# Kernel optimization log

Hardware: AMD Instinct MI355X
Metric: run time of the kernel (lower is better)

The kernel has to match this reference:

```python
import jax, jax.numpy as jnp
import numpy as np

NHEADS = 8
EPS = 1e-6


def setup_inputs() -> dict:
    key = jax.random.key(0)
    ks = jax.random.split(key, 6)
    B, N, H, W = 4, 80, 24, 24
    hidden, guid = 128, 128
    n = B * H * W
    S = 77
    return {
        "query": jax.random.normal(ks[0], (B, N, H, W, hidden + guid), jnp.float32),
        "x": jax.random.normal(ks[1], (n, S, hidden), jnp.float32),
        "guidance": jax.random.normal(ks[2], (n, S, guid), jnp.float32),
        "Wq": jax.random.normal(ks[3], (hidden + guid, hidden), jnp.float32) * (1.0 / np.sqrt(hidden + guid)),
        "bq": jnp.zeros((hidden,), jnp.float32),
        "Wk": jax.random.normal(ks[4], (hidden + guid, hidden), jnp.float32) * (1.0 / np.sqrt(hidden + guid)),
        "bk": jnp.zeros((hidden,), jnp.float32),
        "Wv": jax.random.normal(ks[5], (hidden, hidden), jnp.float32) * (1.0 / np.sqrt(hidden)),
        "bv": jnp.zeros((hidden,), jnp.float32),
    }


def _feature_map(x):
    return jax.nn.elu(x) + 1.0


def reference(query, x, guidance, Wq, bq, Wk, bk, Wv, bv):
    B, N, H, W, C = query.shape
    Dh = Wq.shape[1] // NHEADS  # head dim
    # 'B N H W C -> (B H W) N C'
    qin = query.transpose(0, 2, 3, 1, 4).reshape(B * H * W, N, C)
    q = qin @ Wq + bq                                   # (n, N, hidden)
    k = jnp.concatenate([x, guidance], axis=-1) @ Wk + bk  # (n, S, hidden)
    v = x @ Wv + bv                                     # (n, S, hidden)
    n, S = v.shape[0], v.shape[1]
    q = q.reshape(n, N, NHEADS, Dh)
    k = k.reshape(n, S, NHEADS, Dh)
    v = v.reshape(n, S, NHEADS, Dh)
    Q = _feature_map(q)
    K = _feature_map(k)
    v_scaled = v / S
    KV = jnp.einsum('nshd,nshv->nhdv', K, v_scaled)     # (n, h, d, d)
    Z = 1.0 / (jnp.einsum('nlhd,nhd->nlh', Q, K.sum(axis=1)) + EPS)
    queried = jnp.einsum('nlhd,nhdv,nlh->nlhv', Q, KV, Z) * S  # (n, N, h, d)
    out = queried.mean(axis=1).reshape(n, NHEADS * Dh)  # (n, hidden)
    return out.reshape(B, H, W, NHEADS * Dh)
```

## Files before the change

### kernel.cpp

```cpp
#include <hip/hip_runtime.h>
#include <hip/hip_bf16.h>

typedef __attribute__((ext_vector_type(8))) short bf16x8;
typedef __attribute__((ext_vector_type(4))) float f32x4;

#define S77  77
#define NQ   80
#define CS   136
#define KS2  104

#define MFMA(a,b,c) __builtin_amdgcn_mfma_f32_16x16x32_bf16((a),(b),(c),0,0,0)

__device__ __forceinline__ unsigned int cvt_pk(float a, float b) {
    union { __hip_bfloat162 h; unsigned int u; } c;
    c.h = __float22bfloat162_rn(make_float2(a, b));
    return c.u;
}
__device__ __forceinline__ unsigned short f2bf(float f) {
    union { __hip_bfloat16 h; unsigned short u; } c;
    c.h = __float2bfloat16(f);
    return c.u;
}

__global__ void transpose_weights(const float* __restrict__ Wq,
                                  const float* __restrict__ Wk,
                                  const float* __restrict__ Wv,
                                  unsigned short* __restrict__ ws) {
    int t = blockIdx.x * 256 + threadIdx.x;
    if (t < 32768) {
        int k = t >> 7, c = t & 127;
        ws[c * 256 + k] = f2bf(Wq[t]);
    } else if (t < 65536) {
        int u = t - 32768; int k = u >> 7, c = u & 127;
        ws[32768 + c * 256 + k] = f2bf(Wk[u]);
    } else if (t < 81920) {
        int u = t - 65536; int k = u >> 7, c = u & 127;
        ws[65536 + c * 128 + k] = f2bf(Wv[u]);
    }
}

__global__ __launch_bounds__(512, 4)
void attn_kernel(const float* __restrict__ query,
                 const float* __restrict__ x,
                 const float* __restrict__ guid,
                 const unsigned short* __restrict__ wT,
                 const float* __restrict__ bq,
                 const float* __restrict__ bk,
                 const float* __restrict__ bv,
                 float* __restrict__ out)
{
    const int n    = blockIdx.x;
    const int tid  = threadIdx.x;
    const int wid  = tid >> 6;
    const int lane = tid & 63;
    const int quad = lane >> 4;
    const int mr   = lane & 15;
    const int rg   = wid >> 2;
    const int cg   = wid & 3;
    const int b    = n / 576;
    const int hw   = n % 576;
    const int r0   = rg * 48;

    __shared__ union {
        unsigned short stage[2][96 * CS];
        unsigned short tr[2][128 * KS2];
        float qbar[256];
    } U;
    __shared__ float KsumP[256];

    const unsigned short* WqT = wT;
    const unsigned short* WkT = wT + 32768;
    const unsigned short* WvT = wT + 65536;
    const f32x4 cZ = {0.f, 0.f, 0.f, 0.f};

    const float* xg = x    + (size_t)n * S77 * 128;
    const float* gg = guid + (size_t)n * S77 * 128;

    const int srow = tid >> 5;
    const int seg  = tid & 31;

    float4 sb[5];

    f32x4 Kacc[3][2], Vacc[3][2];
    #pragma unroll
    for (int i = 0; i < 3; ++i) {
        Kacc[i][0] = cZ; Kacc[i][1] = cZ;
        Vacc[i][0] = cZ; Vacc[i][1] = cZ;
    }

    #pragma unroll
    for (int it = 0; it < 5; ++it) {
        const int s = srow + it * 16;
        if (s < S77) sb[it] = *(const float4*)(xg + (size_t)s * 128 + seg * 4);
    }
    #pragma unroll
    for (int it = 0; it < 5; ++it) {
        const int s = srow + it * 16;
        if (s < S77) {
            uint2 p; p.x = cvt_pk(sb[it].x, sb[it].y); p.y = cvt_pk(sb[it].z, sb[it].w);
            *(uint2*)&U.stage[0][s * CS + seg * 4] = p;
        }
    }
    __syncthreads();

    #pragma unroll
    for (int c = 0; c < 2; ++c) {
        if (c == 0) {
            #pragma unroll
            for (int it = 0; it < 5; ++it) {
                const int s = srow + it * 16;
                if (s < S77) sb[it] = *(const float4*)(gg + (size_t)s * 128 + seg * 4);
            }
        }
        const unsigned short* sbase = U.stage[c];
        #pragma unroll
        for (int kk = 0; kk < 4; ++kk) {
            const int kloc  = kk * 32 + quad * 8;
            const int kglob = c * 128 + kk * 32;
            bf16x8 a0 = *(const bf16x8*)&sbase[(r0      + mr) * CS + kloc];
            bf16x8 a1 = *(const bf16x8*)&sbase[(r0 + 16 + mr) * CS + kloc];
            bf16x8 a2;
            if (rg == 0) a2 = *(const bf16x8*)&sbase[(32 + mr) * CS + kloc];
            #pragma unroll
            for (int t = 0; t < 2; ++t) {
                const int cc = cg * 32 + t * 16 + mr;
                bf16x8 bkf = *(const bf16x8*)(WkT + cc * 256 + kglob + quad * 8);
                Kacc[0][t] = MFMA(a0, bkf, Kacc[0][t]);
                Kacc[1][t] = MFMA(a1, bkf, Kacc[1][t]);
                if (rg == 0) Kacc[2][t] = MFMA(a2, bkf, Kacc[2][t]);
                if (c == 0) {
                    bf16x8 bvf = *(const bf16x8*)(WvT + cc * 128 + kglob + quad * 8);
                    Vacc[0][t] = MFMA(a0, bvf, Vacc[0][t]);
                    Vacc[1][t] = MFMA(a1, bvf, Vacc[1][t]);
                    if (rg == 0) Vacc[2][t] = MFMA(a2, bvf, Vacc[2][t]);
                }
            }
        }
        if (c == 0) {
            #pragma unroll
            for (int it = 0; it < 5; ++it) {
                const int s = srow + it * 16;
                if (s < S77) {
                    uint2 p; p.x = cvt_pk(sb[it].x, sb[it].y); p.y = cvt_pk(sb[it].z, sb[it].w);
                    *(uint2*)&U.stage[1][s * CS + seg * 4] = p;
                }
            }
        }
        __syncthreads();
    }

    #pragma unroll
    for (int t = 0; t < 2; ++t) {
        const int cc = cg * 32 + t * 16 + mr;
        const float biask = bk[cc];
        const float biasv = bv[cc];
        float ksp = 0.f;
        #pragma unroll
        for (int mt = 0; mt < 3; ++mt) {
            const int s0 = r0 + mt * 16 + quad * 4;
            float kv4[4], vv4[4];
            #pragma unroll
            for (int r = 0; r < 4; ++r) {
                const int s = s0 + r;
                float tk = 0.f, tv = 0.f;
                if (s < S77) {
                    tk = Kacc[mt][t][r] + biask;
                    tk = (tk > 0.f) ? (tk + 1.f) : __expf(tk);
                    tv = Vacc[mt][t][r] + biasv;
                }
                kv4[r] = tk; vv4[r] = tv; ksp += tk;
            }
            uint2 pk_; pk_.x = cvt_pk(kv4[0], kv4[1]); pk_.y = cvt_pk(kv4[2], kv4[3]);
            *(uint2*)&U.tr[0][cc * KS2 + s0] = pk_;
            uint2 pv_; pv_.x = cvt_pk(vv4[0], vv4[1]); pv_.y = cvt_pk(vv4[2], vv4[3]);
            *(uint2*)&U.tr[1][cc * KS2 + s0] = pv_;
        }
        ksp += __shfl_xor(ksp, 16);
        ksp += __shfl_xor(ksp, 32);
        if (quad == 0) KsumP[rg * 128 + cc] = ksp;
    }

    #pragma unroll
    for (int it = 0; it < 5; ++it) {
        const int l = srow + it * 16;
        sb[it] = *(const float4*)(query + ((size_t)(b * 80 + l) * 576 + hw) * 256 + seg * 4);
    }
    __syncthreads();

    f32x4 KVacc = cZ;
    #pragma unroll
    for (int ks3 = 0; ks3 < 3; ++ks3) {
        const int sc = ks3 * 32 + quad * 8;
        bf16x8 a  = *(const bf16x8*)&U.tr[0][(wid * 16 + mr) * KS2 + sc];
        bf16x8 bb = *(const bf16x8*)&U.tr[1][(wid * 16 + mr) * KS2 + sc];
        KVacc = MFMA(a, bb, KVacc);
    }
    __syncthreads();

    f32x4 Qacc[3][2];
    #pragma unroll
    for (int i = 0; i < 3; ++i) { Qacc[i][0] = cZ; Qacc[i][1] = cZ; }

    #pragma unroll
    for (int it = 0; it < 5; ++it) {
        const int l = srow + it * 16;
        uint2 p; p.x = cvt_pk(sb[it].x, sb[it].y); p.y = cvt_pk(sb[it].z, sb[it].w);
        *(uint2*)&U.stage[0][l * CS + seg * 4] = p;
    }
    __syncthreads();

    #pragma unroll
    for (int c = 0; c < 2; ++c) {
        if (c == 0) {
            #pragma unroll
            for (int it = 0; it < 5; ++it) {
                const int l = srow + it * 16;
                sb[it] = *(const float4*)(query + ((size_t)(b * 80 + l) * 576 + hw) * 256 + 128 + seg * 4);
            }
        }
        const unsigned short* sbase = U.stage[c];
        #pragma unroll
        for (int kk = 0; kk < 4; ++kk) {
            const int kloc  = kk * 32 + quad * 8;
            const int kglob = c * 128 + kk * 32;
            bf16x8 a0 = *(const bf16x8*)&sbase[(r0      + mr) * CS + kloc];
            bf16x8 a1 = *(const bf16x8*)&sbase[(r0 + 16 + mr) * CS + kloc];
            bf16x8 a2;
            if (rg == 0) a2 = *(const bf16x8*)&sbase[(32 + mr) * CS + kloc];
            #pragma unroll
            for (int t = 0; t < 2; ++t) {
                const int cc = cg * 32 + t * 16 + mr;
                bf16x8 bqf = *(const bf16x8*)(WqT + cc * 256 + kglob + quad * 8);
                Qacc[0][t] = MFMA(a0, bqf, Qacc[0][t]);
                Qacc[1][t] = MFMA(a1, bqf, Qacc[1][t]);
                if (rg == 0) Qacc[2][t] = MFMA(a2, bqf, Qacc[2][t]);
            }
        }
        if (c == 0) {
            #pragma unroll
            for (int it = 0; it < 5; ++it) {
                const int l = srow + it * 16;
                uint2 p; p.x = cvt_pk(sb[it].x, sb[it].y); p.y = cvt_pk(sb[it].z, sb[it].w);
                *(uint2*)&U.stage[1][l * CS + seg * 4] = p;
            }
        }
        __syncthreads();
    }

    #pragma unroll
    for (int t = 0; t < 2; ++t) {
        const int cc = cg * 32 + t * 16 + mr;
        const float biasq = bq[cc];
        const float ksc = KsumP[cc] + KsumP[128 + cc];
        float qb = 0.f;
        #pragma unroll
        for (int mt = 0; mt < 3; ++mt) {
            if (!(rg == 1 && mt == 2)) {
                #pragma unroll
                for (int r = 0; r < 4; ++r) {
                    float qv = Qacc[mt][t][r] + biasq;
                    qv = (qv > 0.f) ? (qv + 1.f) : __expf(qv);
                    float den = qv * ksc;
                    den += __shfl_xor(den, 1);
                    den += __shfl_xor(den, 2);
                    den += __shfl_xor(den, 4);
                    den += __shfl_xor(den, 8);
                    qb += qv * (1.f / (den + 1e-6f));
                }
            }
        }
        qb += __shfl_xor(qb, 16);
        qb += __shfl_xor(qb, 32);
        if (quad == 0) U.qbar[rg * 128 + cc] = qb;
    }
    __syncthreads();

    {
        float o = 0.f;
        #pragma unroll
        for (int r = 0; r < 4; ++r) {
            const int d = wid * 16 + quad * 4 + r;
            const float qbar = U.qbar[d] + U.qbar[128 + d];
            o += qbar * KVacc[r];
        }
        o += __shfl_xor(o, 16);
        o += __shfl_xor(o, 32);
        if (quad == 0) out[(size_t)n * 128 + wid * 16 + mr] = o * (1.f / 80.f);
    }
}

extern "C" void kernel_launch(void* const* d_in, const int* in_sizes, int n_in,
                              void* d_out, int out_size, void* d_ws, size_t ws_size,
                              hipStream_t stream) {
    const float* query = (const float*)d_in[0];
    const float* x     = (const float*)d_in[1];
    const float* g     = (const float*)d_in[2];
    const float* Wq    = (const float*)d_in[3];
    const float* bq    = (const float*)d_in[4];
    const float* Wk    = (const float*)d_in[5];
    const float* bk    = (const float*)d_in[6];
    const float* Wv    = (const float*)d_in[7];
    const float* bv    = (const float*)d_in[8];
    float* out = (float*)d_out;
    unsigned short* ws = (unsigned short*)d_ws;

    hipLaunchKernelGGL(transpose_weights, dim3(320), dim3(256), 0, stream, Wq, Wk, Wv, ws);
    hipLaunchKernelGGL(attn_kernel, dim3(2304), dim3(512), 0, stream,
                       query, x, g, ws, bq, bk, bv, out);
}
```

Before: 465.9 us.

## Assign one head per wave and transpose K/V fragments in registers

Work is repartitioned so each of the 8 waves owns one 16-column head across all 80 rows, instead of splitting rows and columns across waves. The K/V transpose for the KV matmul now uses cross-lane shuffles rather than an LDS round trip, and the key sums, qbar and output reductions stay within the wave. This removes the tr/qbar/KsumP shared buffers and several __syncthreads, and weight fragments are preloaded into registers. The cost is more register pressure from 5 row tiles per wave and extra shuffle work.

New measurement: 439.5 us. 1.06x faster.

```diff
diff --git a/kernel.cpp b/kernel.cpp
--- a/kernel.cpp
+++ b/kernel.cpp
@@ -4,10 +4,8 @@
 typedef __attribute__((ext_vector_type(8))) short bf16x8;
 typedef __attribute__((ext_vector_type(4))) float f32x4;
 
-#define S77  77
-#define NQ   80
-#define CS   136
-#define KS2  104
+#define S77 77
+#define CS  136
 
 #define MFMA(a,b,c) __builtin_amdgcn_mfma_f32_16x16x32_bf16((a),(b),(c),0,0,0)
 
@@ -39,6 +37,27 @@
     }
 }
 
+__device__ __forceinline__ bf16x8 xpose_frag(const float t0[4], const float t1[4],
+                                             int quad, int mr) {
+    unsigned int pk[4];
+    #pragma unroll
+    for (int r = 0; r < 4; ++r) pk[r] = cvt_pk(t0[r], t1[r]);
+    const int sb0 = ((quad & 1) * 2) * 16 + mr;
+    unsigned int g0[4], g1[4];
+    #pragma unroll
+    for (int r = 0; r < 4; ++r) {
+        g0[r] = __shfl(pk[r], sb0);
+        g1[r] = __shfl(pk[r], sb0 + 16);
+    }
+    const unsigned int sh = (quad & 2) ? 16u : 0u;
+    union { unsigned int u[4]; bf16x8 v; } o;
+    o.u[0] = ((g0[0] >> sh) & 0xffffu) | (((g0[1] >> sh) & 0xffffu) << 16);
+    o.u[1] = ((g0[2] >> sh) & 0xffffu) | (((g0[3] >> sh) & 0xffffu) << 16);
+    o.u[2] = ((g1[0] >> sh) & 0xffffu) | (((g1[1] >> sh) & 0xffffu) << 16);
+    o.u[3] = ((g1[2] >> sh) & 0xffffu) | (((g1[3] >> sh) & 0xffffu) << 16);
+    return o.v;
+}
+
 __global__ __launch_bounds__(512, 4)
 void attn_kernel(const float* __restrict__ query,
                  const float* __restrict__ x,
@@ -51,22 +70,14 @@
 {
     const int n    = blockIdx.x;
     const int tid  = threadIdx.x;
-    const int wid  = tid >> 6;
+    const int h    = tid >> 6;
     const int lane = tid & 63;
     const int quad = lane >> 4;
     const int mr   = lane & 15;
-    const int rg   = wid >> 2;
-    const int cg   = wid & 3;
     const int b    = n / 576;
     const int hw   = n % 576;
-    const int r0   = rg * 48;
-
-    __shared__ union {
-        unsigned short stage[2][96 * CS];
-        unsigned short tr[2][128 * KS2];
-        float qbar[256];
-    } U;
-    __shared__ float KsumP[256];
+
+    __shared__ unsigned short stage[2][80 * CS];
 
     const unsigned short* WqT = wT;
     const unsigned short* WkT = wT + 32768;
@@ -75,19 +86,20 @@
 
     const float* xg = x    + (size_t)n * S77 * 128;
     const float* gg = guid + (size_t)n * S77 * 128;
-
     const int srow = tid >> 5;
     const int seg  = tid & 31;
 
+    const int cc = h * 16 + mr;
+    const float bk_c = bk[cc], bv_c = bv[cc], bq_c = bq[cc];
+
+    bf16x8 wk0[4], wv0[4];
+    #pragma unroll
+    for (int kk = 0; kk < 4; ++kk) {
+        wk0[kk] = *(const bf16x8*)(WkT + cc * 256 + kk * 32 + quad * 8);
+        wv0[kk] = *(const bf16x8*)(WvT + cc * 128 + kk * 32 + quad * 8);
+    }
+
     float4 sb[5];
-
-    f32x4 Kacc[3][2], Vacc[3][2];
-    #pragma unroll
-    for (int i = 0; i < 3; ++i) {
-        Kacc[i][0] = cZ; Kacc[i][1] = cZ;
-        Vacc[i][0] = cZ; Vacc[i][1] = cZ;
-    }
-
     #pragma unroll
     for (int it = 0; it < 5; ++it) {
         const int s = srow + it * 16;
@@ -98,195 +110,162 @@
         const int s = srow + it * 16;
         if (s < S77) {
             uint2 p; p.x = cvt_pk(sb[it].x, sb[it].y); p.y = cvt_pk(sb[it].z, sb[it].w);
-            *(uint2*)&U.stage[0][s * CS + seg * 4] = p;
-        }
-    }
-    __syncthreads();
-
-    #pragma unroll
-    for (int c = 0; c < 2; ++c) {
-        if (c == 0) {
-            #pragma unroll
-            for (int it = 0; it < 5; ++it) {
-                const int s = srow + it * 16;
-                if (s < S77) sb[it] = *(const float4*)(gg + (size_t)s * 128 + seg * 4);
+            *(uint2*)&stage[0][s * CS + seg * 4] = p;
+        }
+    }
+    #pragma unroll
+    for (int it = 0; it < 5; ++it) {
+        const int s = srow + it * 16;
+        if (s < S77) sb[it] = *(const float4*)(gg + (size_t)s * 128 + seg * 4);
+    }
+    __syncthreads();
+
+    f32x4 Kacc[5], Vacc[5];
+    #pragma unroll
+    for (int m = 0; m < 5; ++m) { Kacc[m] = cZ; Vacc[m] = cZ; }
+    #pragma unroll
+    for (int kk = 0; kk < 4; ++kk)
+        #pragma unroll
+        for (int m = 0; m < 5; ++m) {
+            bf16x8 a = *(const bf16x8*)&stage[0][(m * 16 + mr) * CS + kk * 32 + quad * 8];
+            Kacc[m] = MFMA(a, wk0[kk], Kacc[m]);
+            Vacc[m] = MFMA(a, wv0[kk], Vacc[m]);
+        }
+
+    bf16x8 wk1[4];
+    #pragma unroll
+    for (int kk = 0; kk < 4; ++kk)
+        wk1[kk] = *(const bf16x8*)(WkT + cc * 256 + 128 + kk * 32 + quad * 8);
+
+    #pragma unroll
+    for (int it = 0; it < 5; ++it) {
+        const int s = srow + it * 16;
+        if (s < S77) {
+            uint2 p; p.x = cvt_pk(sb[it].x, sb[it].y); p.y = cvt_pk(sb[it].z, sb[it].w);
+            *(uint2*)&stage[1][s * CS + seg * 4] = p;
+        }
+    }
+    #pragma unroll
+    for (int it = 0; it < 5; ++it) {
+        const int l = srow + it * 16;
+        sb[it] = *(const float4*)(query + ((size_t)(b * 80 + l) * 576 + hw) * 256 + seg * 4);
+    }
+    __syncthreads();
+
+    #pragma unroll
+    for (int kk = 0; kk < 4; ++kk)
+        #pragma unroll
+        for (int m = 0; m < 5; ++m) {
+            bf16x8 a = *(const bf16x8*)&stage[1][(m * 16 + mr) * CS + kk * 32 + quad * 8];
+            Kacc[m] = MFMA(a, wk1[kk], Kacc[m]);
+        }
+
+    float kf[5][4], vs[5][4];
+    float ksum = 0.f;
+    #pragma unroll
+    for (int m = 0; m < 5; ++m)
+        #pragma unroll
+        for (int r = 0; r < 4; ++r) {
+            const int s = m * 16 + quad * 4 + r;
+            float tk = 0.f, tv = 0.f;
+            if (s < S77) {
+                tk = Kacc[m][r] + bk_c;
+                tk = (tk > 0.f) ? (tk + 1.f) : __expf(tk);
+                tv = Vacc[m][r] + bv_c;
             }
-        }
-        const unsigned short* sbase = U.stage[c];
-        #pragma unroll
-        for (int kk = 0; kk < 4; ++kk) {
-            const int kloc  = kk * 32 + quad * 8;
-            const int kglob = c * 128 + kk * 32;
-            bf16x8 a0 = *(const bf16x8*)&sbase[(r0      + mr) * CS + kloc];
-            bf16x8 a1 = *(const bf16x8*)&sbase[(r0 + 16 + mr) * CS + kloc];
-            bf16x8 a2;
-            if (rg == 0) a2 = *(const bf16x8*)&sbase[(32 + mr) * CS + kloc];
-            #pragma unroll
-            for (int t = 0; t < 2; ++t) {
-                const int cc = cg * 32 + t * 16 + mr;
-                bf16x8 bkf = *(const bf16x8*)(WkT + cc * 256 + kglob + quad * 8);
-                Kacc[0][t] = MFMA(a0, bkf, Kacc[0][t]);
-                Kacc[1][t] = MFMA(a1, bkf, Kacc[1][t]);
-                if (rg == 0) Kacc[2][t] = MFMA(a2, bkf, Kacc[2][t]);
-                if (c == 0) {
-                    bf16x8 bvf = *(const bf16x8*)(WvT + cc * 128 + kglob + quad * 8);
-                    Vacc[0][t] = MFMA(a0, bvf, Vacc[0][t]);
-                    Vacc[1][t] = MFMA(a1, bvf, Vacc[1][t]);
-                    if (rg == 0) Vacc[2][t] = MFMA(a2, bvf, Vacc[2][t]);
-                }
-            }
-        }
-        if (c == 0) {
-            #pragma unroll
-            for (int it = 0; it < 5; ++it) {
-                const int s = srow + it * 16;
-                if (s < S77) {
-                    uint2 p; p.x = cvt_pk(sb[it].x, sb[it].y); p.y = cvt_pk(sb[it].z, sb[it].w);
-                    *(uint2*)&U.stage[1][s * CS + seg * 4] = p;
-                }
-            }
-        }
-        __syncthreads();
-    }
-
-    #pragma unroll
-    for (int t = 0; t < 2; ++t) {
-        const int cc = cg * 32 + t * 16 + mr;
-        const float biask = bk[cc];
-        const float biasv = bv[cc];
-        float ksp = 0.f;
-        #pragma unroll
-        for (int mt = 0; mt < 3; ++mt) {
-            const int s0 = r0 + mt * 16 + quad * 4;
-            float kv4[4], vv4[4];
-            #pragma unroll
-            for (int r = 0; r < 4; ++r) {
-                const int s = s0 + r;
-                float tk = 0.f, tv = 0.f;
-                if (s < S77) {
-                    tk = Kacc[mt][t][r] + biask;
-                    tk = (tk > 0.f) ? (tk + 1.f) : __expf(tk);
-                    tv = Vacc[mt][t][r] + biasv;
-                }
-                kv4[r] = tk; vv4[r] = tv; ksp += tk;
-            }
-            uint2 pk_; pk_.x = cvt_pk(kv4[0], kv4[1]); pk_.y = cvt_pk(kv4[2], kv4[3]);
-            *(uint2*)&U.tr[0][cc * KS2 + s0] = pk_;
-            uint2 pv_; pv_.x = cvt_pk(vv4[0], vv4[1]); pv_.y = cvt_pk(vv4[2], vv4[3]);
-            *(uint2*)&U.tr[1][cc * KS2 + s0] = pv_;
-        }
-        ksp += __shfl_xor(ksp, 16);
-        ksp += __shfl_xor(ksp, 32);
-        if (quad == 0) KsumP[rg * 128 + cc] = ksp;
-    }
-
-    #pragma unroll
-    for (int it = 0; it < 5; ++it) {
-        const int l = srow + it * 16;
-        sb[it] = *(const float4*)(query + ((size_t)(b * 80 + l) * 576 + hw) * 256 + seg * 4);
-    }
-    __syncthreads();
-
+            kf[m][r] = tk; vs[m][r] = tv; ksum += tk;
+        }
+    ksum += __shfl_xor(ksum, 16);
+    ksum += __shfl_xor(ksum, 32);
+
+    const float z4[4] = {0.f, 0.f, 0.f, 0.f};
     f32x4 KVacc = cZ;
-    #pragma unroll
-    for (int ks3 = 0; ks3 < 3; ++ks3) {
-        const int sc = ks3 * 32 + quad * 8;
-        bf16x8 a  = *(const bf16x8*)&U.tr[0][(wid * 16 + mr) * KS2 + sc];
-        bf16x8 bb = *(const bf16x8*)&U.tr[1][(wid * 16 + mr) * KS2 + sc];
-        KVacc = MFMA(a, bb, KVacc);
-    }
-    __syncthreads();
-
-    f32x4 Qacc[3][2];
-    #pragma unroll
-    for (int i = 0; i < 3; ++i) { Qacc[i][0] = cZ; Qacc[i][1] = cZ; }
+    {
+        bf16x8 af, bf;
+        af = xpose_frag(kf[0], kf[1], quad, mr);
+        bf = xpose_frag(vs[0], vs[1], quad, mr);
+        KVacc = MFMA(af, bf, KVacc);
+        af = xpose_frag(kf[2], kf[3], quad, mr);
+        bf = xpose_frag(vs[2], vs[3], quad, mr);
+        KVacc = MFMA(af, bf, KVacc);
+        af = xpose_frag(kf[4], z4, quad, mr);
+        bf = xpose_frag(vs[4], z4, quad, mr);
+        KVacc = MFMA(af, bf, KVacc);
+    }
 
     #pragma unroll
     for (int it = 0; it < 5; ++it) {
         const int l = srow + it * 16;
         uint2 p; p.x = cvt_pk(sb[it].x, sb[it].y); p.y = cvt_pk(sb[it].z, sb[it].w);
-        *(uint2*)&U.stage[0][l * CS + seg * 4] = p;
-    }
-    __syncthreads();
-
-    #pragma unroll
-    for (int c = 0; c < 2; ++c) {
-        if (c == 0) {
-            #pragma unroll
-            for (int it = 0; it < 5; ++it) {
-                const int l = srow + it * 16;
-                sb[it] = *(const float4*)(query + ((size_t)(b * 80 + l) * 576 + hw) * 256 + 128 + seg * 4);
-            }
-        }
-        const unsigned short* sbase = U.stage[c];
-        #pragma unroll
-        for (int kk = 0; kk < 4; ++kk) {
-            const int kloc  = kk * 32 + quad * 8;
-            const int kglob = c * 128 + kk * 32;
-            bf16x8 a0 = *(const bf16x8*)&sbase[(r0      + mr) * CS + kloc];
-            bf16x8 a1 = *(const bf16x8*)&sbase[(r0 + 16 + mr) * CS + kloc];
-            bf16x8 a2;
-            if (rg == 0) a2 = *(const bf16x8*)&sbase[(32 + mr) * CS + kloc];
-            #pragma unroll
-            for (int t = 0; t < 2; ++t) {
-                const int cc = cg * 32 + t * 16 + mr;
-                bf16x8 bqf = *(const bf16x8*)(WqT + cc * 256 + kglob + quad * 8);
-                Qacc[0][t] = MFMA(a0, bqf, Qacc[0][t]);
-                Qacc[1][t] = MFMA(a1, bqf, Qacc[1][t]);
-                if (rg == 0) Qacc[2][t] = MFMA(a2, bqf, Qacc[2][t]);
-            }
-        }
-        if (c == 0) {
-            #pragma unroll
-            for (int it = 0; it < 5; ++it) {
-                const int l = srow + it * 16;
-                uint2 p; p.x = cvt_pk(sb[it].x, sb[it].y); p.y = cvt_pk(sb[it].z, sb[it].w);
-                *(uint2*)&U.stage[1][l * CS + seg * 4] = p;
-            }
-        }
-        __syncthreads();
-    }
-
-    #pragma unroll
-    for (int t = 0; t < 2; ++t) {
-        const int cc = cg * 32 + t * 16 + mr;
-        const float biasq = bq[cc];
-        const float ksc = KsumP[cc] + KsumP[128 + cc];
-        float qb = 0.f;
-        #pragma unroll
-        for (int mt = 0; mt < 3; ++mt) {
-            if (!(rg == 1 && mt == 2)) {
-                #pragma unroll
-                for (int r = 0; r < 4; ++r) {
-                    float qv = Qacc[mt][t][r] + biasq;
-                    qv = (qv > 0.f) ? (qv + 1.f) : __expf(qv);
-                    float den = qv * ksc;
-                    den += __shfl_xor(den, 1);
-                    den += __shfl_xor(den, 2);
-                    den += __shfl_xor(den, 4);
-                    den += __shfl_xor(den, 8);
-                    qb += qv * (1.f / (den + 1e-6f));
-                }
-            }
-        }
-        qb += __shfl_xor(qb, 16);
-        qb += __shfl_xor(qb, 32);
-        if (quad == 0) U.qbar[rg * 128 + cc] = qb;
-    }
-    __syncthreads();
-
-    {
-        float o = 0.f;
+        *(uint2*)&stage[0][l * CS + seg * 4] = p;
+    }
+    #pragma unroll
+    for (int it = 0; it < 5; ++it) {
+        const int l = srow + it * 16;
+        sb[it] = *(const float4*)(query + ((size_t)(b * 80 + l) * 576 + hw) * 256 + 128 + seg * 4);
+    }
+    bf16x8 wq0[4];
+    #pragma unroll
+    for (int kk = 0; kk < 4; ++kk)
+        wq0[kk] = *(const bf16x8*)(WqT + cc * 256 + kk * 32 + quad * 8);
+    __syncthreads();
+
+    f32x4 Qacc[5];
+    #pragma unroll
+    for (int m = 0; m < 5; ++m) Qacc[m] = cZ;
+    #pragma unroll
+    for (int kk = 0; kk < 4; ++kk)
+        #pragma unroll
+        for (int m = 0; m < 5; ++m) {
+            bf16x8 a = *(const bf16x8*)&stage[0][(m * 16 + mr) * CS + kk * 32 + quad * 8];
+            Qacc[m] = MFMA(a, wq0[kk], Qacc[m]);
+        }
+    bf16x8 wq1[4];
+    #pragma unroll
+    for (int kk = 0; kk < 4; ++kk)
+        wq1[kk] = *(const bf16x8*)(WqT + cc * 256 + 128 + kk * 32 + quad * 8);
+    #pragma unroll
+    for (int it = 0; it < 5; ++it) {
+        const int l = srow + it * 16;
+        uint2 p; p.x = cvt_pk(sb[it].x, sb[it].y); p.y = cvt_pk(sb[it].z, sb[it].w);
+        *(uint2*)&stage[1][l * CS + seg * 4] = p;
+    }
+    __syncthreads();
+
+    #pragma unroll
+    for (int kk = 0; kk < 4; ++kk)
+        #pragma unroll
+        for (int m = 0; m < 5; ++m) {
+            bf16x8 a = *(const bf16x8*)&stage[1][(m * 16 + mr) * CS + kk * 32 + quad * 8];
+            Qacc[m] = MFMA(a, wq1[kk], Qacc[m]);
+        }
+
+    float qbar = 0.f;
+    #pragma unroll
+    for (int m = 0; m < 5; ++m)
         #pragma unroll
         for (int r = 0; r < 4; ++r) {
-            const int d = wid * 16 + quad * 4 + r;
-            const float qbar = U.qbar[d] + U.qbar[128 + d];
-            o += qbar * KVacc[r];
-        }
-        o += __shfl_xor(o, 16);
-        o += __shfl_xor(o, 32);
-        if (quad == 0) out[(size_t)n * 128 + wid * 16 + mr] = o * (1.f / 80.f);
-    }
+            float qv = Qacc[m][r] + bq_c;
+            qv = (qv > 0.f) ? (qv + 1.f) : __expf(qv);
+            float den = qv * ksum;
+            den += __shfl_xor(den, 1);
+            den += __shfl_xor(den, 2);
+            den += __shfl_xor(den, 4);
+            den += __shfl_xor(den, 8);
+            qbar += qv * (1.f / (den + 1e-6f));
+        }
+    qbar += __shfl_xor(qbar, 16);
+    qbar += __shfl_xor(qbar, 32);
+
+    float o = 0.f;
+    #pragma unroll
+    for (int r = 0; r < 4; ++r) {
+        const float qb_r = __shfl(qbar, quad * 4 + r);
+        o += qb_r * KVacc[r];
+    }
+    o += __shfl_xor(o, 16);
+    o += __shfl_xor(o, 32);
+    if (quad == 0) out[(size_t)n * 128 + cc] = o * (1.f / 80.f);
 }
 
 extern "C" void kernel_launch(void* const* d_in, const int* in_sizes, int n_in,
```
